# Optimization experiments

Measured on AMD Instinct MI355X. Metric: run time of the kernel, lower is better.

## Reference

```python
import jax, jax.numpy as jnp
import numpy as np

T, N = 256, 128
STATE_D, TARGET_D = 64, 64
HID = 512
A, P = 8, 8
AP = A * P
REPEAT = 2
THR = 1.0  # snntorch default threshold


@jax.custom_vjp
def spike(x):
    # Heaviside with ATan surrogate gradient (snntorch default, alpha=2)
    return (x > 0.0).astype(x.dtype)

def _spike_fwd(x):
    return (x > 0.0).astype(x.dtype), x

def _spike_bwd(x, g):
    return (g / (1.0 + (jnp.pi * x) ** 2),)

spike.defvjp(_spike_fwd, _spike_bwd)


def setup_inputs() -> dict:
    key = jax.random.key(0)
    ks = jax.random.split(key, 16)
    in_dim = STATE_D + TARGET_D
    g = lambda k, shape, fan: (jax.random.uniform(k, shape, jnp.float32) * 2.0 - 1.0) / np.sqrt(fan)
    return {
        "state": jax.random.normal(ks[0], (T, N, STATE_D), jnp.float32),
        "target": jax.random.normal(ks[1], (T, N, TARGET_D), jnp.float32),
        "W_rec_in": g(ks[2], (HID, in_dim), in_dim),
        "b_rec_in": jnp.zeros((HID,), jnp.float32),
        "W_rec": g(ks[3], (HID, HID), HID),
        "b_rec": jnp.zeros((HID,), jnp.float32),
        "alpha_rec": jax.random.uniform(ks[4], (HID,), jnp.float32),
        "beta_rec": jax.random.uniform(ks[5], (HID,), jnp.float32),
        "W_ff_in": g(ks[6], (HID, HID), HID),
        "b_ff_in": jnp.zeros((HID,), jnp.float32),
        "alpha_ff": jax.random.uniform(ks[7], (HID,), jnp.float32),
        "beta_ff": jax.random.uniform(ks[8], (HID,), jnp.float32),
        "W_mu_in": g(ks[9], (AP, HID), HID),
        "b_mu_in": jnp.zeros((AP,), jnp.float32),
        "beta_mu": jax.random.uniform(ks[10], (AP,), jnp.float32),
        "W_mu_out": jnp.full((A, AP), 1.0 / P, jnp.float32),
        "W_lv_in": g(ks[11], (AP, HID), HID),
        "b_lv_in": jnp.zeros((AP,), jnp.float32),
        "beta_lv": jax.random.uniform(ks[12], (AP,), jnp.float32),
        "W_lv_out": jnp.full((A, AP), 1.0 / P, jnp.float32),
    }


def _forward(state, target, W_rec_in, b_rec_in, W_rec, b_rec, alpha_rec, beta_rec,
             W_ff_in, b_ff_in, alpha_ff, beta_ff,
             W_mu_in, b_mu_in, beta_mu, W_mu_out,
             W_lv_in, b_lv_in, beta_lv, W_lv_out):
    x_all = jnp.concatenate([state, target], axis=-1)  # [T, N, in_dim]

    def neuron_step(carry, x):
        spk_r, syn_r, mem_r, syn_f, mem_f, mem_mu, mem_lv = carry
        # --- RSynaptic (recurrent LIF with synaptic current), reset=subtract ---
        cur_r = x @ W_rec_in.T + b_rec_in + spk_r @ W_rec.T + b_rec
        reset_r = jax.lax.stop_gradient((mem_r > THR).astype(x.dtype))
        syn_r = alpha_rec * syn_r + cur_r
        mem_r = beta_rec * mem_r + syn_r - reset_r * THR
        spk_r = spike(mem_r - THR)
        # --- Synaptic feed-forward layer, reset=subtract ---
        cur_f = spk_r @ W_ff_in.T + b_ff_in
        reset_f = jax.lax.stop_gradient((mem_f > THR).astype(x.dtype))
        syn_f = alpha_ff * syn_f + cur_f
        mem_f = beta_ff * mem_f + syn_f - reset_f * THR
        spk_f = spike(mem_f - THR)
        # --- readout Synaptic neurons: alpha=0 (syn == input), reset='none' ---
        mem_mu = beta_mu * mem_mu + (spk_f @ W_mu_in.T + b_mu_in)
        mem_lv = beta_lv * mem_lv + (spk_f @ W_lv_in.T + b_lv_in)
        mu = mem_mu @ W_mu_out.T   # [N, A]
        lv = mem_lv @ W_lv_out.T   # [N, A]
        return (spk_r, syn_r, mem_r, syn_f, mem_f, mem_mu, mem_lv), (mu, lv)

    def t_step(carry, x):
        mus, lvs = [], []
        for _ in range(REPEAT):  # repeat_input, fixed and small
            carry, (mu, lv) = neuron_step(carry, x)
            mus.append(mu)
            lvs.append(lv)
        return carry, (jnp.mean(jnp.stack(mus), 0), jnp.mean(jnp.stack(lvs), 0))

    z = jnp.zeros((N, HID), state.dtype)
    z2 = jnp.zeros((N, AP), state.dtype)
    carry0 = (z, z, z, z, z, z2, z2)
    _, (mu_outs, lv_outs) = jax.lax.scan(t_step, carry0, x_all)
    return mu_outs, lv_outs  # each [T, N, A]


def reference(state, target, W_rec_in, b_rec_in, W_rec, b_rec, alpha_rec, beta_rec,
              W_ff_in, b_ff_in, alpha_ff, beta_ff,
              W_mu_in, b_mu_in, beta_mu, W_mu_out,
              W_lv_in, b_lv_in, beta_lv, W_lv_out):
    return _forward(state, target, W_rec_in, b_rec_in, W_rec, b_rec, alpha_rec, beta_rec,
                    W_ff_in, b_ff_in, alpha_ff, beta_ff,
                    W_mu_in, b_mu_in, beta_mu, W_mu_out,
                    W_lv_in, b_lv_in, beta_lv, W_lv_out)
```

## Files before the change

kernel.cpp:

```cpp
#include <hip/hip_runtime.h>


typedef unsigned int       u32;
typedef unsigned short     u16;
typedef unsigned long long u64;
typedef unsigned char      u8;

#define TSTEPS 512
#define HIDDEN 512

#define XW_OFF    0ull
#define C3_OFF    0ull
#define MEM_OFF   33554432ull
#define SPKB_OFF  100663296ull
#define WT_OFF    109051904ull
#define WINT_OFF  109314048ull
#define RING_OFF  134217728ull
#define CNT_OFF   134742016ull
#define WS_NEED   (134742016ull + 4096ull)

#define QCHUNK 384

__global__ __launch_bounds__(256) void k_prepT(
    const float* __restrict__ Win,
    const float* __restrict__ Wmu, const float* __restrict__ Wlv,
    float* __restrict__ WinT, float* __restrict__ WT)
{
  const int idx = blockIdx.x * 256 + threadIdx.x;
  if (idx < 65536) {
    const int k = idx >> 9, j = idx & 511;
    WinT[idx] = Win[j * 128 + k];
  } else {
    const int i2 = idx - 65536;
    const int k = i2 >> 7, j = i2 & 127;
    WT[i2] = (j < 64) ? Wmu[j * 512 + k] : Wlv[(j - 64) * 512 + k];
  }
}

__global__ __launch_bounds__(256) void k_xw(
    const float* __restrict__ state, const float* __restrict__ target,
    const float* __restrict__ WinT, const float* __restrict__ b_in,
    float* __restrict__ XW)
{
  __shared__ float xs[16][129];
  const int tid  = threadIdx.x;
  const int row0 = blockIdx.x * 16;

  for (int e = tid; e < 2048; e += 256) {
    int r = e >> 7, k = e & 127;
    xs[r][k] = (k < 64) ? state[(row0 + r) * 64 + k]
                        : target[(row0 + r) * 64 + k - 64];
  }
  __syncthreads();

#pragma unroll
  for (int jh = 0; jh < 2; ++jh) {
    const int j = jh * 256 + tid;
    float acc[16];
#pragma unroll
    for (int r = 0; r < 16; ++r) acc[r] = 0.0f;
    for (int k = 0; k < 128; ++k) {
      const float wv = WinT[k * 512 + j];
#pragma unroll
      for (int r = 0; r < 16; ++r)
        acc[r] = __builtin_fmaf(xs[r][k], wv, acc[r]);
    }
    const float b = b_in[j];
#pragma unroll
    for (int r = 0; r < 16; ++r)
      XW[(row0 + r) * 512 + j] = __fadd_rn(acc[r], b);
  }
}

__global__ __launch_bounds__(512, 2) void k_rec(
    const float* __restrict__ XW,
    const float* __restrict__ Wrec, const float* __restrict__ Wff,
    const float* __restrict__ alpha_rec, const float* __restrict__ beta_rec,
    const float* __restrict__ b_rec,
    const float* __restrict__ b_ff, const float* __restrict__ alpha_ff,
    const float* __restrict__ beta_ff,
    u32* __restrict__ ring32, u32* __restrict__ spkb32)
{
  __shared__ float WR[16 * 516];
  __shared__ float WF[16 * 516];
  __shared__ u32   BitsW[2][16][17];

  const int tid  = threadIdx.x;
  const int g    = blockIdx.x & 7;
  const int c    = blockIdx.x >> 3;
  const int n0   = g * 16;
  const int wv   = tid >> 6;
  const int lane = tid & 63;
  const int ch   = lane & 15;
  const int rloc = lane >> 4;
  const int row  = (wv & 3) * 4 + rloc;
  const bool isFF = (wv >= 4);
  const int jj   = c * 16 + ch;

  for (int it = tid; it < 2048; it += 512) {
    const int r16 = it >> 7, k4 = (it & 127) * 4;
    *(float4*)(WR + r16 * 516 + k4) = *(const float4*)(Wrec + (c * 16 + r16) * 512 + k4);
    *(float4*)(WF + r16 * 516 + k4) = *(const float4*)(Wff  + (c * 16 + r16) * 512 + k4);
  }

  float coA, coB, coC;
  if (!isFF) { coA = alpha_rec[jj]; coB = beta_rec[jj]; coC = b_rec[jj]; }
  else       { coA = alpha_ff[jj];  coB = beta_ff[jj];  coC = b_ff[jj]; }

  float syn = 0.f, mem = 0.f, spk = 0.f, xw = 0.f;

  const float* wp = (isFF ? WF : WR) + ch * 516;
  const int srow = tid >> 5;
  const int sjl  = tid & 31;

  __syncthreads();

  for (int tp = 0; tp <= TSTEPS; ++tp) {
    if (!isFF && tp < TSTEPS && !(tp & 1))
      xw = XW[((tp >> 1) * 128 + n0 + row) * 512 + jj];

    float SA = 0.f;

    if (tp > 0) {
      const int bp = (tp - 1) & 1;
      {
        const u32 expct = (u32)tp;
        const u32* src = ring32 + (bp * 128 + n0 + srow) * 32 + sjl;
        u32 m = __hip_atomic_load(src, __ATOMIC_RELAXED, __HIP_MEMORY_SCOPE_AGENT);
        while ((m >> 16) != expct) {
          __builtin_amdgcn_s_sleep(1);
          m = __hip_atomic_load(src, __ATOMIC_RELAXED, __HIP_MEMORY_SCOPE_AGENT);
        }
        ((u16*)BitsW[bp][srow])[sjl] = (u16)m;
      }
      __syncthreads();

      if (isFF || tp < TSTEPS) {
        float aA = 0.f, aB = 0.f;
        for (int kb = 0; kb < 12; ++kb) {
          const u32 w0 = BitsW[bp][row][kb];
#pragma unroll
          for (int k4 = 0; k4 < 32; k4 += 4) {
            const float4 w4 = *(const float4*)(wp + kb * 32 + k4);
#pragma unroll
            for (int i = 0; i < 4; ++i) {
              const float wvv = (i == 0) ? w4.x : (i == 1) ? w4.y : (i == 2) ? w4.z : w4.w;
              aA = __builtin_fmaf((float)((w0 >> (k4 + i)) & 1u), wvv, aA);
            }
          }
        }
        for (int kb = 12; kb < 16; ++kb) {
          const u32 w0 = BitsW[bp][row][kb];
#pragma unroll
          for (int k4 = 0; k4 < 32; k4 += 4) {
            const float4 w4 = *(const float4*)(wp + kb * 32 + k4);
#pragma unroll
            for (int i = 0; i < 4; ++i) {
              const float wvv = (i == 0) ? w4.x : (i == 1) ? w4.y : (i == 2) ? w4.z : w4.w;
              aB = __builtin_fmaf((float)((w0 >> (k4 + i)) & 1u), wvv, aB);
            }
          }
        }
        SA = __fadd_rn(aA, aB);
      }
    }

    if (isFF) {
      if (tp > 0) {
        float curf = __fadd_rn(SA, coC);
        syn = __fadd_rn(__fmul_rn(coA, syn), curf);
        mem = __fsub_rn(__fadd_rn(__fmul_rn(coB, mem), syn), spk);
        spk = (mem > 1.0f) ? 1.0f : 0.0f;
        const u64 B = __ballot(spk != 0.f);
        if (ch == 0) {
          spkb32[((u64)(tp - 1) * 128 + n0 + row) * 32 + c] =
              (u32)((B >> (16 * rloc)) & 0xFFFFull);
        }
      }
    } else {
      if (tp < TSTEPS) {
        float cur = __fadd_rn(__fadd_rn(xw, SA), coC);
        syn = __fadd_rn(__fmul_rn(coA, syn), cur);
        mem = __fsub_rn(__fadd_rn(__fmul_rn(coB, mem), syn), spk);
        spk = (mem > 1.0f) ? 1.0f : 0.0f;
        const u64 B = __ballot(spk != 0.f);
        if (ch == 0) {
          const u32 tag = ((u32)(tp + 1)) << 16;
          __hip_atomic_store(ring32 + ((tp & 1) * 128 + n0 + row) * 32 + c,
                             tag | (u32)((B >> (16 * rloc)) & 0xFFFFull),
                             __ATOMIC_RELAXED, __HIP_MEMORY_SCOPE_AGENT);
        }
      }
    }
  }
}

__global__ __launch_bounds__(256) void k_c3(
    const u32* __restrict__ spkb32, const float* __restrict__ WT,
    const float* __restrict__ bmu, const float* __restrict__ blv,
    float* __restrict__ c3)
{
  __shared__ u32 Bc[32][32];
  const int tid  = threadIdx.x;
  const int rows0 = blockIdx.x * 32;

  for (int it = tid; it < 1024; it += 256)
    ((u32*)Bc)[it] = spkb32[(u64)rows0 * 32 + it];
  __syncthreads();

  const int j  = tid & 127;
  const int rh = tid >> 7;
  const float bias = (j < 64) ? bmu[j] : blv[j - 64];

  float accA[16], accB[16];
#pragma unroll
  for (int r = 0; r < 16; ++r) { accA[r] = 0.f; accB[r] = 0.f; }

  for (int m = 0; m < 24; ++m) {
    u32 wrow[16];
#pragma unroll
    for (int r = 0; r < 16; ++r) wrow[r] = Bc[rh * 16 + r][m];
    const float* wpp = WT + (m * 16) * 128 + j;
#pragma unroll
    for (int kk = 0; kk < 16; ++kk) {
      const float wvv = wpp[kk * 128];
#pragma unroll
      for (int r = 0; r < 16; ++r) {
        const float b = (float)((wrow[r] >> kk) & 1u);
        accA[r] = __builtin_fmaf(b, wvv, accA[r]);
      }
    }
  }
  for (int m = 24; m < 32; ++m) {
    u32 wrow[16];
#pragma unroll
    for (int r = 0; r < 16; ++r) wrow[r] = Bc[rh * 16 + r][m];
    const float* wpp = WT + (m * 16) * 128 + j;
#pragma unroll
    for (int kk = 0; kk < 16; ++kk) {
      const float wvv = wpp[kk * 128];
#pragma unroll
      for (int r = 0; r < 16; ++r) {
        const float b = (float)((wrow[r] >> kk) & 1u);
        accB[r] = __builtin_fmaf(b, wvv, accB[r]);
      }
    }
  }

#pragma unroll
  for (int r = 0; r < 16; ++r)
    c3[(u64)(rows0 + rh * 16 + r) * 128 + j] =
        __fadd_rn(__fadd_rn(accA[r], accB[r]), bias);
}

__global__ __launch_bounds__(256) void k_scan(
    const float* __restrict__ c3,
    const float* __restrict__ beta_mu, const float* __restrict__ beta_lv,
    float* __restrict__ Mem)
{
  const int tid = blockIdx.x * 256 + threadIdx.x;
  const int n = tid >> 7, ap = tid & 127;
  const float beta = (ap < 64) ? beta_mu[ap] : beta_lv[ap - 64];
  const float* src = c3 + n * 128 + ap;
  float* dst = Mem + n * 128 + ap;
  float mem = 0.0f;
  for (int t = 0; t < 512; ++t) {
    mem = __fadd_rn(__fmul_rn(beta, mem), src[(u64)t * 16384]);
    dst[(u64)t * 16384] = mem;
  }
}

__global__ __launch_bounds__(256) void k_out(
    const float* __restrict__ Mem,
    const float* __restrict__ Wmu_out, const float* __restrict__ Wlv_out,
    float* __restrict__ out)
{
  const int tid = blockIdx.x * 256 + threadIdx.x;
  const int a = tid & 7;
  const int n = (tid >> 3) & 127;
  const int t = (tid >> 10) & 255;
  const int kind = tid >> 18;
  const float* wv = ((kind == 0) ? Wmu_out : Wlv_out) + a * 64;
  const float* s0 = Mem + ((u64)(2 * t) * 128 + n) * 128 + kind * 64;
  const float* s1 = Mem + ((u64)(2 * t + 1) * 128 + n) * 128 + kind * 64;
  float mu0 = 0.0f, mu1 = 0.0f;
#pragma unroll 8
  for (int q = 0; q < 64; ++q) mu0 = __builtin_fmaf(s0[q], wv[q], mu0);
#pragma unroll 8
  for (int q = 0; q < 64; ++q) mu1 = __builtin_fmaf(s1[q], wv[q], mu1);
  out[tid] = __fmul_rn(__fadd_rn(mu0, mu1), 0.5f);
}

extern "C" void kernel_launch(void* const* d_in, const int* in_sizes, int n_in,
                              void* d_out, int out_size, void* d_ws, size_t ws_size,
                              hipStream_t stream) {
  (void)in_sizes; (void)n_in; (void)out_size;
  if (ws_size < WS_NEED) return;

  const float* state     = (const float*)d_in[0];
  const float* target    = (const float*)d_in[1];
  const float* W_rec_in  = (const float*)d_in[2];
  const float* b_rec_in  = (const float*)d_in[3];
  const float* W_rec     = (const float*)d_in[4];
  const float* b_rec     = (const float*)d_in[5];
  const float* alpha_rec = (const float*)d_in[6];
  const float* beta_rec  = (const float*)d_in[7];
  const float* W_ff_in   = (const float*)d_in[8];
  const float* b_ff_in   = (const float*)d_in[9];
  const float* alpha_ff  = (const float*)d_in[10];
  const float* beta_ff   = (const float*)d_in[11];
  const float* W_mu_in   = (const float*)d_in[12];
  const float* b_mu_in   = (const float*)d_in[13];
  const float* beta_mu   = (const float*)d_in[14];
  const float* W_mu_out  = (const float*)d_in[15];
  const float* W_lv_in   = (const float*)d_in[16];
  const float* b_lv_in   = (const float*)d_in[17];
  const float* beta_lv   = (const float*)d_in[18];
  const float* W_lv_out  = (const float*)d_in[19];

  char* ws = (char*)d_ws;
  float* XW    = (float*)(ws + XW_OFF);
  float* c3    = (float*)(ws + C3_OFF);
  float* Mem   = (float*)(ws + MEM_OFF);
  u32*   spkb32= (u32*)  (ws + SPKB_OFF);
  float* WT    = (float*)(ws + WT_OFF);
  float* WinT  = (float*)(ws + WINT_OFF);
  u32*   ring32= (u32*)  (ws + RING_OFF);

  hipLaunchKernelGGL(k_prepT, dim3(512), dim3(256), 0, stream,
                     W_rec_in, W_mu_in, W_lv_in, WinT, WT);
  hipLaunchKernelGGL(k_xw, dim3(2048), dim3(256), 0, stream,
                     state, target, WinT, b_rec_in, XW);
  hipLaunchKernelGGL(k_rec, dim3(256), dim3(512), 0, stream,
                     XW, W_rec, W_ff_in,
                     alpha_rec, beta_rec, b_rec,
                     b_ff_in, alpha_ff, beta_ff, ring32, spkb32);
  hipLaunchKernelGGL(k_c3, dim3(2048), dim3(256), 0, stream,
                     spkb32, WT, b_mu_in, b_lv_in, c3);
  hipLaunchKernelGGL(k_scan, dim3(64), dim3(256), 0, stream,
                     c3, beta_mu, beta_lv, Mem);
  hipLaunchKernelGGL(k_out, dim3(2048), dim3(256), 0, stream,
                     Mem, W_mu_out, W_lv_out, (float*)d_out);
}
```

Before: 4.152 ms.

## Restructure recurrent kernel: register-resident weights, readlane bit-masked sums, per-step ring

Rewrites the persistent recurrent spiking kernel so each thread holds an 8-weight slice in registers and broadcasts weights with readlane. It replaces the bit-to-float FMAs with masked adds over spike bitmasks. Blocks now each own 8 neurons for 64 batch rows, with separate blocks for the recurrent and feed-forward layers. A full-length per-timestep ring of 8-bit tagged spike masks replaces the double-buffered 16-bit ring. The input projection is stored transposed for coalesced per-step loads, and the readout kernel is adapted to the byte-packed spike layout. This trades shared-memory weight reads for unrolled readlane and ALU work, adds more polling loads per step, and needs a larger workspace for the ring.

```diff
diff --git a/kernel.cpp b/kernel.cpp
--- a/kernel.cpp
+++ b/kernel.cpp
@@ -12,14 +12,11 @@
 #define XW_OFF    0ull
 #define C3_OFF    0ull
 #define MEM_OFF   33554432ull
+#define RINGN_OFF 67108864ull
 #define SPKB_OFF  100663296ull
 #define WT_OFF    109051904ull
 #define WINT_OFF  109314048ull
-#define RING_OFF  134217728ull
-#define CNT_OFF   134742016ull
 #define WS_NEED   (134742016ull + 4096ull)
-
-#define QCHUNK 384
 
 __global__ __launch_bounds__(256) void k_prepT(
     const float* __restrict__ Win,
@@ -40,7 +37,7 @@
 __global__ __launch_bounds__(256) void k_xw(
     const float* __restrict__ state, const float* __restrict__ target,
     const float* __restrict__ WinT, const float* __restrict__ b_in,
-    float* __restrict__ XW)
+    float* __restrict__ XWT)
 {
   __shared__ float xs[16][129];
   const int tid  = threadIdx.x;
@@ -53,6 +50,9 @@
   }
   __syncthreads();
 
+  const int t2 = row0 >> 7;
+  const int n0 = row0 & 127;
+
 #pragma unroll
   for (int jh = 0; jh < 2; ++jh) {
     const int j = jh * 256 + tid;
@@ -66,146 +66,147 @@
         acc[r] = __builtin_fmaf(xs[r][k], wv, acc[r]);
     }
     const float b = b_in[j];
-#pragma unroll
-    for (int r = 0; r < 16; ++r)
-      XW[(row0 + r) * 512 + j] = __fadd_rn(acc[r], b);
+    float* dst = XWT + ((u64)t2 * 512 + j) * 128 + n0;
+#pragma unroll
+    for (int r4 = 0; r4 < 4; ++r4) {
+      float4 o;
+      o.x = __fadd_rn(acc[r4 * 4 + 0], b);
+      o.y = __fadd_rn(acc[r4 * 4 + 1], b);
+      o.z = __fadd_rn(acc[r4 * 4 + 2], b);
+      o.w = __fadd_rn(acc[r4 * 4 + 3], b);
+      *(float4*)(dst + r4 * 4) = o;
+    }
   }
 }
 
 __global__ __launch_bounds__(512, 2) void k_rec(
-    const float* __restrict__ XW,
+    const float* __restrict__ XWT,
     const float* __restrict__ Wrec, const float* __restrict__ Wff,
     const float* __restrict__ alpha_rec, const float* __restrict__ beta_rec,
     const float* __restrict__ b_rec,
     const float* __restrict__ b_ff, const float* __restrict__ alpha_ff,
     const float* __restrict__ beta_ff,
-    u32* __restrict__ ring32, u32* __restrict__ spkb32)
-{
-  __shared__ float WR[16 * 516];
-  __shared__ float WF[16 * 516];
-  __shared__ u32   BitsW[2][16][17];
+    u32* __restrict__ ring32, u8* __restrict__ spkb8)
+{
+  __shared__ __align__(16) u8 MB[64][80];
+  __shared__ __align__(8)  u8 SP[64][8];
 
   const int tid  = threadIdx.x;
-  const int g    = blockIdx.x & 7;
-  const int c    = blockIdx.x >> 3;
-  const int n0   = g * 16;
-  const int wv   = tid >> 6;
-  const int lane = tid & 63;
-  const int ch   = lane & 15;
-  const int rloc = lane >> 4;
-  const int row  = (wv & 3) * 4 + rloc;
-  const bool isFF = (wv >= 4);
-  const int jj   = c * 16 + ch;
-
-  for (int it = tid; it < 2048; it += 512) {
-    const int r16 = it >> 7, k4 = (it & 127) * 4;
-    *(float4*)(WR + r16 * 516 + k4) = *(const float4*)(Wrec + (c * 16 + r16) * 512 + k4);
-    *(float4*)(WF + r16 * 516 + k4) = *(const float4*)(Wff  + (c * 16 + r16) * 512 + k4);
-  }
-
-  float coA, coB, coC;
-  if (!isFF) { coA = alpha_rec[jj]; coB = beta_rec[jj]; coC = b_rec[jj]; }
-  else       { coA = alpha_ff[jj];  coB = beta_ff[jj];  coC = b_ff[jj]; }
+  const int w    = tid >> 6;
+  const int n    = tid & 63;
+  const int bb   = blockIdx.x & 127;
+  const bool isFF = (blockIdx.x >= 128);
+  const int cb   = bb >> 1;
+  const int R    = bb & 1;
+  const int jj   = cb * 8 + w;
+  const int gn   = R * 64 + n;
+
+  const float* Wbase = (isFF ? Wff : Wrec) + (u64)jj * 512 + n * 8;
+  const float4 wv0 = *(const float4*)(Wbase + 0);
+  const float4 wv1 = *(const float4*)(Wbase + 4);
+  int wd[8];
+  wd[0] = __float_as_int(wv0.x); wd[1] = __float_as_int(wv0.y);
+  wd[2] = __float_as_int(wv0.z); wd[3] = __float_as_int(wv0.w);
+  wd[4] = __float_as_int(wv1.x); wd[5] = __float_as_int(wv1.y);
+  wd[6] = __float_as_int(wv1.z); wd[7] = __float_as_int(wv1.w);
+
+  const float coA = isFF ? alpha_ff[jj] : alpha_rec[jj];
+  const float coB = isFF ? beta_ff[jj]  : beta_rec[jj];
+  const float coC = isFF ? b_ff[jj]     : b_rec[jj];
 
   float syn = 0.f, mem = 0.f, spk = 0.f, xw = 0.f;
 
-  const float* wp = (isFF ? WF : WR) + ch * 516;
-  const int srow = tid >> 5;
-  const int sjl  = tid & 31;
-
-  __syncthreads();
-
-  for (int tp = 0; tp <= TSTEPS; ++tp) {
-    if (!isFF && tp < TSTEPS && !(tp & 1))
-      xw = XW[((tp >> 1) * 128 + n0 + row) * 512 + jj];
+#pragma unroll 1
+  for (int i = 0; i < TSTEPS; ++i) {
+    asm volatile("" : "+v"(wd[0]), "+v"(wd[1]), "+v"(wd[2]), "+v"(wd[3]),
+                      "+v"(wd[4]), "+v"(wd[5]), "+v"(wd[6]), "+v"(wd[7]));
+
+    if (!isFF && !(i & 1))
+      xw = XWT[((u64)(i >> 1) * 512 + jj) * 128 + gn];
+
+    const int slot  = isFF ? i : (i - 1);
+    const u32 expct = isFF ? (u32)(i + 1) : (u32)i;
+
+    if (expct) {
+      const u32* src = ring32 + ((u64)slot * 64 + 8 * w) * 128 + gn;
+      u32 vv[8];
+      for (;;) {
+        u32 bad = 0;
+#pragma unroll
+        for (int s = 0; s < 8; ++s) {
+          vv[s] = __hip_atomic_load(src + s * 128, __ATOMIC_RELAXED,
+                                    __HIP_MEMORY_SCOPE_AGENT);
+          bad |= (vv[s] >> 8) ^ expct;
+        }
+        if (__all(bad == 0)) break;
+        __builtin_amdgcn_s_sleep(1);
+      }
+      u64 mb = 0;
+#pragma unroll
+      for (int s = 0; s < 8; ++s) mb |= (u64)(vv[s] & 0xFFu) << (8 * s);
+      *(u64*)&MB[n][8 * w] = mb;
+    }
+    __syncthreads();
 
     float SA = 0.f;
-
-    if (tp > 0) {
-      const int bp = (tp - 1) & 1;
-      {
-        const u32 expct = (u32)tp;
-        const u32* src = ring32 + (bp * 128 + n0 + srow) * 32 + sjl;
-        u32 m = __hip_atomic_load(src, __ATOMIC_RELAXED, __HIP_MEMORY_SCOPE_AGENT);
-        while ((m >> 16) != expct) {
-          __builtin_amdgcn_s_sleep(1);
-          m = __hip_atomic_load(src, __ATOMIC_RELAXED, __HIP_MEMORY_SCOPE_AGENT);
-        }
-        ((u16*)BitsW[bp][srow])[sjl] = (u16)m;
-      }
-      __syncthreads();
-
-      if (isFF || tp < TSTEPS) {
-        float aA = 0.f, aB = 0.f;
-        for (int kb = 0; kb < 12; ++kb) {
-          const u32 w0 = BitsW[bp][row][kb];
-#pragma unroll
-          for (int k4 = 0; k4 < 32; k4 += 4) {
-            const float4 w4 = *(const float4*)(wp + kb * 32 + k4);
-#pragma unroll
-            for (int i = 0; i < 4; ++i) {
-              const float wvv = (i == 0) ? w4.x : (i == 1) ? w4.y : (i == 2) ? w4.z : w4.w;
-              aA = __builtin_fmaf((float)((w0 >> (k4 + i)) & 1u), wvv, aA);
-            }
-          }
-        }
-        for (int kb = 12; kb < 16; ++kb) {
-          const u32 w0 = BitsW[bp][row][kb];
-#pragma unroll
-          for (int k4 = 0; k4 < 32; k4 += 4) {
-            const float4 w4 = *(const float4*)(wp + kb * 32 + k4);
-#pragma unroll
-            for (int i = 0; i < 4; ++i) {
-              const float wvv = (i == 0) ? w4.x : (i == 1) ? w4.y : (i == 2) ? w4.z : w4.w;
-              aB = __builtin_fmaf((float)((w0 >> (k4 + i)) & 1u), wvv, aB);
-            }
-          }
-        }
-        SA = __fadd_rn(aA, aB);
-      }
-    }
-
-    if (isFF) {
-      if (tp > 0) {
-        float curf = __fadd_rn(SA, coC);
-        syn = __fadd_rn(__fmul_rn(coA, syn), curf);
-        mem = __fsub_rn(__fadd_rn(__fmul_rn(coB, mem), syn), spk);
-        spk = (mem > 1.0f) ? 1.0f : 0.0f;
-        const u64 B = __ballot(spk != 0.f);
-        if (ch == 0) {
-          spkb32[((u64)(tp - 1) * 128 + n0 + row) * 32 + c] =
-              (u32)((B >> (16 * rloc)) & 0xFFFFull);
-        }
-      }
-    } else {
-      if (tp < TSTEPS) {
-        float cur = __fadd_rn(__fadd_rn(xw, SA), coC);
-        syn = __fadd_rn(__fmul_rn(coA, syn), cur);
-        mem = __fsub_rn(__fadd_rn(__fmul_rn(coB, mem), syn), spk);
-        spk = (mem > 1.0f) ? 1.0f : 0.0f;
-        const u64 B = __ballot(spk != 0.f);
-        if (ch == 0) {
-          const u32 tag = ((u32)(tp + 1)) << 16;
-          __hip_atomic_store(ring32 + ((tp & 1) * 128 + n0 + row) * 32 + c,
-                             tag | (u32)((B >> (16 * rloc)) & 0xFFFFull),
-                             __ATOMIC_RELAXED, __HIP_MEMORY_SCOPE_AGENT);
-        }
+    if (expct) {
+      const uint4* bq = (const uint4*)&MB[n][0];
+      const uint4 q0 = bq[0], q1 = bq[1], q2 = bq[2], q3 = bq[3];
+      u32 b[16] = { q0.x, q0.y, q0.z, q0.w, q1.x, q1.y, q1.z, q1.w,
+                    q2.x, q2.y, q2.z, q2.w, q3.x, q3.y, q3.z, q3.w };
+      float aA = 0.f, aB = 0.f;
+#pragma unroll
+      for (int k = 0; k < 512; ++k) {
+        const int wq  = __builtin_amdgcn_readlane(wd[k & 7], k >> 3);
+        const int msk = (int)(b[k >> 5] << (31 - (k & 31))) >> 31;
+        const float ws = __int_as_float(msk & wq);
+        if (k < 384) aA = __fadd_rn(aA, ws);
+        else         aB = __fadd_rn(aB, ws);
+      }
+      SA = __fadd_rn(aA, aB);
+    }
+
+    const float cur = isFF ? __fadd_rn(SA, coC)
+                           : __fadd_rn(__fadd_rn(xw, SA), coC);
+    syn = __fadd_rn(__fmul_rn(coA, syn), cur);
+    mem = __fsub_rn(__fadd_rn(__fmul_rn(coB, mem), syn), spk);
+    spk = (mem > 1.0f) ? 1.0f : 0.0f;
+    SP[n][w] = (u8)(spk != 0.f);
+
+    __syncthreads();
+
+    if (w == 0) {
+      const u64 sv  = *(const u64*)&SP[n][0];
+      const u32 lo4 = ((u32)sv         * 0x01020408u) >> 24;
+      const u32 hi4 = ((u32)(sv >> 32) * 0x01020408u) >> 24;
+      const u32 mask = lo4 | (hi4 << 4);
+      if (!isFF) {
+        __hip_atomic_store(ring32 + ((u64)i * 64 + cb) * 128 + gn,
+                           ((u32)(i + 1) << 8) | mask,
+                           __ATOMIC_RELAXED, __HIP_MEMORY_SCOPE_AGENT);
+      } else {
+        spkb8[((u64)i * 64 + cb) * 128 + gn] = (u8)mask;
       }
     }
   }
 }
 
 __global__ __launch_bounds__(256) void k_c3(
-    const u32* __restrict__ spkb32, const float* __restrict__ WT,
+    const u8* __restrict__ spkb8, const float* __restrict__ WT,
     const float* __restrict__ bmu, const float* __restrict__ blv,
     float* __restrict__ c3)
 {
-  __shared__ u32 Bc[32][32];
-  const int tid  = threadIdx.x;
+  __shared__ __align__(8) u8 Bc[64][40];
+  const int tid   = threadIdx.x;
   const int rows0 = blockIdx.x * 32;
-
-  for (int it = tid; it < 1024; it += 256)
-    ((u32*)Bc)[it] = spkb32[(u64)rows0 * 32 + it];
+  const int t     = rows0 >> 7;
+  const int n0    = rows0 & 127;
+
+  {
+    const int c8 = tid >> 2, g = tid & 3;
+    const u64 vv = *(const u64*)(spkb8 + ((u64)t * 64 + c8) * 128 + n0 + 8 * g);
+    *(u64*)&Bc[c8][8 * g] = vv;
+  }
   __syncthreads();
 
   const int j  = tid & 127;
@@ -216,32 +217,32 @@
 #pragma unroll
   for (int r = 0; r < 16; ++r) { accA[r] = 0.f; accB[r] = 0.f; }
 
-  for (int m = 0; m < 24; ++m) {
-    u32 wrow[16];
-#pragma unroll
-    for (int r = 0; r < 16; ++r) wrow[r] = Bc[rh * 16 + r][m];
-    const float* wpp = WT + (m * 16) * 128 + j;
-#pragma unroll
-    for (int kk = 0; kk < 16; ++kk) {
+  for (int m = 0; m < 48; ++m) {
+    u32 w32[4];
+#pragma unroll
+    for (int q = 0; q < 4; ++q) w32[q] = *(const u32*)&Bc[m][rh * 16 + 4 * q];
+    const float* wpp = WT + (m * 8) * 128 + j;
+#pragma unroll
+    for (int kk = 0; kk < 8; ++kk) {
       const float wvv = wpp[kk * 128];
 #pragma unroll
       for (int r = 0; r < 16; ++r) {
-        const float b = (float)((wrow[r] >> kk) & 1u);
+        const float b = (float)((w32[r >> 2] >> (((r & 3) << 3) + kk)) & 1u);
         accA[r] = __builtin_fmaf(b, wvv, accA[r]);
       }
     }
   }
-  for (int m = 24; m < 32; ++m) {
-    u32 wrow[16];
-#pragma unroll
-    for (int r = 0; r < 16; ++r) wrow[r] = Bc[rh * 16 + r][m];
-    const float* wpp = WT + (m * 16) * 128 + j;
-#pragma unroll
-    for (int kk = 0; kk < 16; ++kk) {
+  for (int m = 48; m < 64; ++m) {
+    u32 w32[4];
+#pragma unroll
+    for (int q = 0; q < 4; ++q) w32[q] = *(const u32*)&Bc[m][rh * 16 + 4 * q];
+    const float* wpp = WT + (m * 8) * 128 + j;
+#pragma unroll
+    for (int kk = 0; kk < 8; ++kk) {
       const float wvv = wpp[kk * 128];
 #pragma unroll
       for (int r = 0; r < 16; ++r) {
-        const float b = (float)((wrow[r] >> kk) & 1u);
+        const float b = (float)((w32[r >> 2] >> (((r & 3) << 3) + kk)) & 1u);
         accB[r] = __builtin_fmaf(b, wvv, accB[r]);
       }
     }
@@ -319,24 +320,24 @@
   const float* W_lv_out  = (const float*)d_in[19];
 
   char* ws = (char*)d_ws;
-  float* XW    = (float*)(ws + XW_OFF);
+  float* XWT   = (float*)(ws + XW_OFF);
   float* c3    = (float*)(ws + C3_OFF);
   float* Mem   = (float*)(ws + MEM_OFF);
-  u32*   spkb32= (u32*)  (ws + SPKB_OFF);
+  u32*   ring32= (u32*)  (ws + RINGN_OFF);
+  u8*    spkb8 = (u8*)   (ws + SPKB_OFF);
   float* WT    = (float*)(ws + WT_OFF);
   float* WinT  = (float*)(ws + WINT_OFF);
-  u32*   ring32= (u32*)  (ws + RING_OFF);
 
   hipLaunchKernelGGL(k_prepT, dim3(512), dim3(256), 0, stream,
                      W_rec_in, W_mu_in, W_lv_in, WinT, WT);
   hipLaunchKernelGGL(k_xw, dim3(2048), dim3(256), 0, stream,
-                     state, target, WinT, b_rec_in, XW);
+                     state, target, WinT, b_rec_in, XWT);
   hipLaunchKernelGGL(k_rec, dim3(256), dim3(512), 0, stream,
-                     XW, W_rec, W_ff_in,
+                     XWT, W_rec, W_ff_in,
                      alpha_rec, beta_rec, b_rec,
-                     b_ff_in, alpha_ff, beta_ff, ring32, spkb32);
+                     b_ff_in, alpha_ff, beta_ff, ring32, spkb8);
   hipLaunchKernelGGL(k_c3, dim3(2048), dim3(256), 0, stream,
-                     spkb32, WT, b_mu_in, b_lv_in, c3);
+                     spkb8, WT, b_mu_in, b_lv_in, c3);
   hipLaunchKernelGGL(k_scan, dim3(64), dim3(256), 0, stream,
                      c3, beta_mu, beta_lv, Mem);
   hipLaunchKernelGGL(k_out, dim3(2048), dim3(256), 0, stream,
```

Measured after the change: 5.417 ms. 1.3x slower.

## Split recurrent and feedforward layers into separate blocks with a spike history buffer

Applied to the files above, without the earlier changes.

The recurrent kernel now gives each block either the recurrent or the feedforward layer over 32 output columns, instead of both layers over 16 columns. The feedforward blocks read recurrent spikes from a per-timestep history buffer. This lets the feedforward layer trail the recurrent chain instead of sitting inside its critical loop. The inner product replaces the float conversion plus FMA with a sign-extended bitmask AND feeding an add, and spike bits are stored as 16-bit words. The cost is two memsets per call, an 8 MB history buffer, and extra polling traffic from the feedforward blocks.

```diff
diff --git a/kernel.cpp b/kernel.cpp
--- a/kernel.cpp
+++ b/kernel.cpp
@@ -12,14 +12,14 @@
 #define XW_OFF    0ull
 #define C3_OFF    0ull
 #define MEM_OFF   33554432ull
-#define SPKB_OFF  100663296ull
+#define RING_OFF  67108864ull
+#define HIST_OFF  68157440ull
+#define SPKB_OFF  83886080ull
 #define WT_OFF    109051904ull
 #define WINT_OFF  109314048ull
-#define RING_OFF  134217728ull
-#define CNT_OFF   134742016ull
 #define WS_NEED   (134742016ull + 4096ull)
 
-#define QCHUNK 384
+#define WSTRIDE 514
 
 __global__ __launch_bounds__(256) void k_prepT(
     const float* __restrict__ Win,
@@ -68,7 +68,7 @@
     const float b = b_in[j];
 #pragma unroll
     for (int r = 0; r < 16; ++r)
-      XW[(row0 + r) * 512 + j] = __fadd_rn(acc[r], b);
+      XW[(u64)(row0 + r) * 512 + j] = __fadd_rn(acc[r], b);
   }
 }
 
@@ -79,133 +79,171 @@
     const float* __restrict__ b_rec,
     const float* __restrict__ b_ff, const float* __restrict__ alpha_ff,
     const float* __restrict__ beta_ff,
-    u32* __restrict__ ring32, u32* __restrict__ spkb32)
-{
-  __shared__ float WR[16 * 516];
-  __shared__ float WF[16 * 516];
-  __shared__ u32   BitsW[2][16][17];
+    u32* __restrict__ ring32, u32* __restrict__ hist32,
+    u16* __restrict__ spkb16)
+{
+  __shared__ __align__(16) float WL[32 * WSTRIDE];
+  __shared__ __align__(16) u16 MB[2][16][32];
+  __shared__ float padlds[3584];
 
   const int tid  = threadIdx.x;
-  const int g    = blockIdx.x & 7;
-  const int c    = blockIdx.x >> 3;
-  const int n0   = g * 16;
-  const int wv   = tid >> 6;
-  const int lane = tid & 63;
-  const int ch   = lane & 15;
-  const int rloc = lane >> 4;
-  const int row  = (wv & 3) * 4 + rloc;
-  const bool isFF = (wv >= 4);
-  const int jj   = c * 16 + ch;
-
-  for (int it = tid; it < 2048; it += 512) {
-    const int r16 = it >> 7, k4 = (it & 127) * 4;
-    *(float4*)(WR + r16 * 516 + k4) = *(const float4*)(Wrec + (c * 16 + r16) * 512 + k4);
-    *(float4*)(WF + r16 * 516 + k4) = *(const float4*)(Wff  + (c * 16 + r16) * 512 + k4);
-  }
-
-  float coA, coB, coC;
-  if (!isFF) { coA = alpha_rec[jj]; coB = beta_rec[jj]; coC = b_rec[jj]; }
-  else       { coA = alpha_ff[jj];  coB = beta_ff[jj];  coC = b_ff[jj]; }
+  const int w    = tid >> 6;
+  const int l    = tid & 63;
+  const bool isFF = (blockIdx.x >= 128);
+  const int bb   = blockIdx.x & 127;
+  const int rg   = bb >> 4;
+  const int c    = bb & 15;
+  const int u    = l & 31;
+  const int rp   = l >> 5;
+  const int rl   = 2 * w + rp;
+  const int g    = 16 * rg + rl;
+  const int jj   = 32 * c + u;
+  const int widx = l & 31;
+
+  {
+    const float* Wsrc = isFF ? Wff : Wrec;
+    for (int it = tid; it < 8192; it += 512) {
+      const int uu = it >> 8, m2 = (it & 255) * 2;
+      *(float2*)(WL + uu * WSTRIDE + m2) =
+          *(const float2*)(Wsrc + (u64)(32 * c + uu) * 512 + m2);
+    }
+  }
+
+  const float coA = isFF ? alpha_ff[jj] : alpha_rec[jj];
+  const float coB = isFF ? beta_ff[jj]  : beta_rec[jj];
+  const float coC = isFF ? b_ff[jj]     : b_rec[jj];
+
+  ((volatile float*)padlds)[tid] = coC;
+
+  const float* WLrow = WL + u * WSTRIDE;
 
   float syn = 0.f, mem = 0.f, spk = 0.f, xw = 0.f;
 
-  const float* wp = (isFF ? WF : WR) + ch * 516;
-  const int srow = tid >> 5;
-  const int sjl  = tid & 31;
-
   __syncthreads();
 
-  for (int tp = 0; tp <= TSTEPS; ++tp) {
-    if (!isFF && tp < TSTEPS && !(tp & 1))
-      xw = XW[((tp >> 1) * 128 + n0 + row) * 512 + jj];
+#pragma unroll 1
+  for (int s = 0; s < TSTEPS; ++s) {
+    const bool doMac = isFF || (s > 0);
+    const int p = isFF ? (s & 1) : ((s - 1) & 1);
+
+    if (doMac) {
+      u32 v;
+      if (!isFF) {
+        const u32 expct = (u32)s;
+        const u32* src = ring32 + p * 4096 + g * 32 + widx;
+        v = __hip_atomic_load(src, __ATOMIC_RELAXED, __HIP_MEMORY_SCOPE_AGENT);
+        while ((v >> 16) != expct) {
+          __builtin_amdgcn_s_sleep(1);
+          v = __hip_atomic_load(src, __ATOMIC_RELAXED, __HIP_MEMORY_SCOPE_AGENT);
+        }
+      } else {
+        const u32 expct = (u32)(s + 1);
+        const u32* src = hist32 + (u64)s * 4096 + g * 32 + widx;
+        v = __hip_atomic_load(src, __ATOMIC_RELAXED, __HIP_MEMORY_SCOPE_AGENT);
+        while ((v >> 16) != expct) {
+          __builtin_amdgcn_s_sleep(1);
+          v = __hip_atomic_load(src, __ATOMIC_RELAXED, __HIP_MEMORY_SCOPE_AGENT);
+        }
+      }
+      MB[p][rl][widx] = (u16)v;
+    }
+
+    if (!isFF && !(s & 1))
+      xw = XW[((u64)(s >> 1) * 128 + g) * 512 + jj];
 
     float SA = 0.f;
-
-    if (tp > 0) {
-      const int bp = (tp - 1) & 1;
-      {
-        const u32 expct = (u32)tp;
-        const u32* src = ring32 + (bp * 128 + n0 + srow) * 32 + sjl;
-        u32 m = __hip_atomic_load(src, __ATOMIC_RELAXED, __HIP_MEMORY_SCOPE_AGENT);
-        while ((m >> 16) != expct) {
-          __builtin_amdgcn_s_sleep(1);
-          m = __hip_atomic_load(src, __ATOMIC_RELAXED, __HIP_MEMORY_SCOPE_AGENT);
+    if (doMac) {
+      const uint4* bq = (const uint4*)&MB[p][rl][0];
+      const uint4 q0 = bq[0], q1 = bq[1], q2 = bq[2], q3 = bq[3];
+      const u32 bw[16] = { q0.x, q0.y, q0.z, q0.w, q1.x, q1.y, q1.z, q1.w,
+                           q2.x, q2.y, q2.z, q2.w, q3.x, q3.y, q3.z, q3.w };
+      float aA = 0.f, aB = 0.f;
+#pragma unroll
+      for (int d = 0; d < 12; ++d) {
+        const int word = (int)bw[d];
+#pragma unroll
+        for (int k4 = 0; k4 < 32; k4 += 4) {
+          const float2 wa = *(const float2*)(WLrow + d * 32 + k4);
+          const float2 wb = *(const float2*)(WLrow + d * 32 + k4 + 2);
+          aA = __fadd_rn(aA, __int_as_float(
+              __builtin_amdgcn_sbfe(word, k4 + 0, 1) & __float_as_int(wa.x)));
+          aA = __fadd_rn(aA, __int_as_float(
+              __builtin_amdgcn_sbfe(word, k4 + 1, 1) & __float_as_int(wa.y)));
+          aA = __fadd_rn(aA, __int_as_float(
+              __builtin_amdgcn_sbfe(word, k4 + 2, 1) & __float_as_int(wb.x)));
+          aA = __fadd_rn(aA, __int_as_float(
+              __builtin_amdgcn_sbfe(word, k4 + 3, 1) & __float_as_int(wb.y)));
         }
-        ((u16*)BitsW[bp][srow])[sjl] = (u16)m;
-      }
-      __syncthreads();
-
-      if (isFF || tp < TSTEPS) {
-        float aA = 0.f, aB = 0.f;
-        for (int kb = 0; kb < 12; ++kb) {
-          const u32 w0 = BitsW[bp][row][kb];
-#pragma unroll
-          for (int k4 = 0; k4 < 32; k4 += 4) {
-            const float4 w4 = *(const float4*)(wp + kb * 32 + k4);
-#pragma unroll
-            for (int i = 0; i < 4; ++i) {
-              const float wvv = (i == 0) ? w4.x : (i == 1) ? w4.y : (i == 2) ? w4.z : w4.w;
-              aA = __builtin_fmaf((float)((w0 >> (k4 + i)) & 1u), wvv, aA);
-            }
-          }
+      }
+#pragma unroll
+      for (int d = 12; d < 16; ++d) {
+        const int word = (int)bw[d];
+#pragma unroll
+        for (int k4 = 0; k4 < 32; k4 += 4) {
+          const float2 wa = *(const float2*)(WLrow + d * 32 + k4);
+          const float2 wb = *(const float2*)(WLrow + d * 32 + k4 + 2);
+          aB = __fadd_rn(aB, __int_as_float(
+              __builtin_amdgcn_sbfe(word, k4 + 0, 1) & __float_as_int(wa.x)));
+          aB = __fadd_rn(aB, __int_as_float(
+              __builtin_amdgcn_sbfe(word, k4 + 1, 1) & __float_as_int(wa.y)));
+          aB = __fadd_rn(aB, __int_as_float(
+              __builtin_amdgcn_sbfe(word, k4 + 2, 1) & __float_as_int(wb.x)));
+          aB = __fadd_rn(aB, __int_as_float(
+              __builtin_amdgcn_sbfe(word, k4 + 3, 1) & __float_as_int(wb.y)));
         }
-        for (int kb = 12; kb < 16; ++kb) {
-          const u32 w0 = BitsW[bp][row][kb];
-#pragma unroll
-          for (int k4 = 0; k4 < 32; k4 += 4) {
-            const float4 w4 = *(const float4*)(wp + kb * 32 + k4);
-#pragma unroll
-            for (int i = 0; i < 4; ++i) {
-              const float wvv = (i == 0) ? w4.x : (i == 1) ? w4.y : (i == 2) ? w4.z : w4.w;
-              aB = __builtin_fmaf((float)((w0 >> (k4 + i)) & 1u), wvv, aB);
-            }
-          }
-        }
-        SA = __fadd_rn(aA, aB);
-      }
-    }
-
-    if (isFF) {
-      if (tp > 0) {
-        float curf = __fadd_rn(SA, coC);
-        syn = __fadd_rn(__fmul_rn(coA, syn), curf);
-        mem = __fsub_rn(__fadd_rn(__fmul_rn(coB, mem), syn), spk);
-        spk = (mem > 1.0f) ? 1.0f : 0.0f;
-        const u64 B = __ballot(spk != 0.f);
-        if (ch == 0) {
-          spkb32[((u64)(tp - 1) * 128 + n0 + row) * 32 + c] =
-              (u32)((B >> (16 * rloc)) & 0xFFFFull);
-        }
+      }
+      SA = __fadd_rn(aA, aB);
+    }
+
+    const float cur = isFF ? __fadd_rn(SA, coC)
+                           : __fadd_rn(__fadd_rn(xw, SA), coC);
+    syn = __fadd_rn(__fmul_rn(coA, syn), cur);
+    mem = __fsub_rn(__fadd_rn(__fmul_rn(coB, mem), syn), spk);
+    spk = (mem > 1.0f) ? 1.0f : 0.0f;
+
+    const u64 B = __ballot(spk != 0.f);
+    if (!isFF) {
+      if (l < 4) {
+        const u32 word = (u32)(B >> (16 * l)) & 0xFFFFu;
+        const int gs = 16 * rg + 2 * w + (l >> 1);
+        const int wx = 2 * c + (l & 1);
+        __hip_atomic_store(ring32 + (s & 1) * 4096 + gs * 32 + wx,
+                           ((u32)(s + 1) << 16) | word,
+                           __ATOMIC_RELAXED, __HIP_MEMORY_SCOPE_AGENT);
+      } else if (l < 8) {
+        const int l2 = l - 4;
+        const u32 word = (u32)(B >> (16 * l2)) & 0xFFFFu;
+        const int gs = 16 * rg + 2 * w + (l2 >> 1);
+        const int wx = 2 * c + (l2 & 1);
+        __hip_atomic_store(hist32 + (u64)s * 4096 + gs * 32 + wx,
+                           ((u32)(s + 1) << 16) | word,
+                           __ATOMIC_RELAXED, __HIP_MEMORY_SCOPE_AGENT);
       }
     } else {
-      if (tp < TSTEPS) {
-        float cur = __fadd_rn(__fadd_rn(xw, SA), coC);
-        syn = __fadd_rn(__fmul_rn(coA, syn), cur);
-        mem = __fsub_rn(__fadd_rn(__fmul_rn(coB, mem), syn), spk);
-        spk = (mem > 1.0f) ? 1.0f : 0.0f;
-        const u64 B = __ballot(spk != 0.f);
-        if (ch == 0) {
-          const u32 tag = ((u32)(tp + 1)) << 16;
-          __hip_atomic_store(ring32 + ((tp & 1) * 128 + n0 + row) * 32 + c,
-                             tag | (u32)((B >> (16 * rloc)) & 0xFFFFull),
-                             __ATOMIC_RELAXED, __HIP_MEMORY_SCOPE_AGENT);
-        }
+      if (l < 4) {
+        const u32 word = (u32)(B >> (16 * l)) & 0xFFFFu;
+        const int gs = 16 * rg + 2 * w + (l >> 1);
+        const int wx = 2 * c + (l & 1);
+        spkb16[(u64)s * 4096 + gs * 32 + wx] = (u16)word;
       }
     }
   }
 }
 
 __global__ __launch_bounds__(256) void k_c3(
-    const u32* __restrict__ spkb32, const float* __restrict__ WT,
+    const u16* __restrict__ spkb16, const float* __restrict__ WT,
     const float* __restrict__ bmu, const float* __restrict__ blv,
     float* __restrict__ c3)
 {
-  __shared__ u32 Bc[32][32];
-  const int tid  = threadIdx.x;
+  __shared__ __align__(8) u16 Bc[32][36];
+  const int tid   = threadIdx.x;
   const int rows0 = blockIdx.x * 32;
 
-  for (int it = tid; it < 1024; it += 256)
-    ((u32*)Bc)[it] = spkb32[(u64)rows0 * 32 + it];
+  {
+    const int r = tid >> 3, gq = tid & 7;
+    const u64 vv = *(const u64*)(spkb16 + (u64)(rows0 + r) * 32 + 4 * gq);
+    *(u64*)&Bc[r][4 * gq] = vv;
+  }
   __syncthreads();
 
   const int j  = tid & 127;
@@ -216,11 +254,11 @@
 #pragma unroll
   for (int r = 0; r < 16; ++r) { accA[r] = 0.f; accB[r] = 0.f; }
 
-  for (int m = 0; m < 24; ++m) {
-    u32 wrow[16];
-#pragma unroll
-    for (int r = 0; r < 16; ++r) wrow[r] = Bc[rh * 16 + r][m];
-    const float* wpp = WT + (m * 16) * 128 + j;
+  for (int wi = 0; wi < 24; ++wi) {
+    u16 wrow[16];
+#pragma unroll
+    for (int r = 0; r < 16; ++r) wrow[r] = Bc[rh * 16 + r][wi];
+    const float* wpp = WT + (wi * 16) * 128 + j;
 #pragma unroll
     for (int kk = 0; kk < 16; ++kk) {
       const float wvv = wpp[kk * 128];
@@ -231,11 +269,11 @@
       }
     }
   }
-  for (int m = 24; m < 32; ++m) {
-    u32 wrow[16];
-#pragma unroll
-    for (int r = 0; r < 16; ++r) wrow[r] = Bc[rh * 16 + r][m];
-    const float* wpp = WT + (m * 16) * 128 + j;
+  for (int wi = 24; wi < 32; ++wi) {
+    u16 wrow[16];
+#pragma unroll
+    for (int r = 0; r < 16; ++r) wrow[r] = Bc[rh * 16 + r][wi];
+    const float* wpp = WT + (wi * 16) * 128 + j;
 #pragma unroll
     for (int kk = 0; kk < 16; ++kk) {
       const float wvv = wpp[kk * 128];
@@ -322,10 +360,14 @@
   float* XW    = (float*)(ws + XW_OFF);
   float* c3    = (float*)(ws + C3_OFF);
   float* Mem   = (float*)(ws + MEM_OFF);
-  u32*   spkb32= (u32*)  (ws + SPKB_OFF);
+  u32*   ring32= (u32*)  (ws + RING_OFF);
+  u32*   hist32= (u32*)  (ws + HIST_OFF);
+  u16*   spkb16= (u16*)  (ws + SPKB_OFF);
   float* WT    = (float*)(ws + WT_OFF);
   float* WinT  = (float*)(ws + WINT_OFF);
-  u32*   ring32= (u32*)  (ws + RING_OFF);
+
+  hipMemsetAsync(ws + RING_OFF, 0, 32768, stream);
+  hipMemsetAsync(ws + HIST_OFF, 0, 8388608, stream);
 
   hipLaunchKernelGGL(k_prepT, dim3(512), dim3(256), 0, stream,
                      W_rec_in, W_mu_in, W_lv_in, WinT, WT);
@@ -334,9 +376,9 @@
   hipLaunchKernelGGL(k_rec, dim3(256), dim3(512), 0, stream,
                      XW, W_rec, W_ff_in,
                      alpha_rec, beta_rec, b_rec,
-                     b_ff_in, alpha_ff, beta_ff, ring32, spkb32);
+                     b_ff_in, alpha_ff, beta_ff, ring32, hist32, spkb16);
   hipLaunchKernelGGL(k_c3, dim3(2048), dim3(256), 0, stream,
-                     spkb32, WT, b_mu_in, b_lv_in, c3);
+                     spkb16, WT, b_mu_in, b_lv_in, c3);
   hipLaunchKernelGGL(k_scan, dim3(64), dim3(256), 0, stream,
                      c3, beta_mu, beta_lv, Mem);
   hipLaunchKernelGGL(k_out, dim3(2048), dim3(256), 0, stream,
```

After: 4.546 ms. 9.5% more time.
